# Optimization experiments

Measured on AMD Instinct MI355X. Metric: run time of the kernel, lower is better.

The kernel has to match this reference:

```python
import jax, jax.numpy as jnp
import numpy as np

D_MODEL = 128
D_STATE = 16
D_CONV = 2
EXPAND = 2
D_INNER = EXPAND * D_MODEL  # 256
DT_RANK = (D_MODEL + 15) // 16  # 8
GROUPS = 4
EPS = 1e-5


def setup_inputs() -> dict:
    key = jax.random.key(0)
    ks = jax.random.split(key, 12)
    s = lambda k, shape, sc=0.02: jax.random.normal(k, shape, dtype=jnp.float32) * sc
    inp = {
        "x_hsi": jax.random.normal(ks[0], (8, D_MODEL, 64, 64), dtype=jnp.float32),
        "W_in": s(ks[1], (D_MODEL, 2 * D_INNER)),            # in_proj (no bias)
        "conv_w": s(ks[2], (D_INNER, D_CONV), 0.5),          # depthwise causal conv, k=2
        "conv_b": s(ks[3], (D_INNER,), 0.1),
        "W_x": s(ks[4], (D_INNER, DT_RANK + 2 * D_STATE)),   # x_proj (no bias)
        "W_dt": s(ks[5], (DT_RANK, D_INNER), 0.1),
        "b_dt": s(ks[6], (D_INNER,), 0.1),
        "A_log": jnp.log(jnp.broadcast_to(jnp.arange(1, D_STATE + 1, dtype=jnp.float32), (D_INNER, D_STATE))),
        "D": jnp.ones((D_INNER,), dtype=jnp.float32),
        "W_out": s(ks[7], (D_INNER, D_MODEL)),               # out_proj (no bias)
        "gn_gamma": jnp.ones((D_MODEL,), dtype=jnp.float32),
        "gn_beta": jnp.zeros((D_MODEL,), dtype=jnp.float32),
    }
    return inp


def _causal_conv_k2(x, w, b):
    # x: [B, L, Din]; w: [Din, 2]; causal depthwise conv, kernel size 2
    xp = jnp.pad(x, ((0, 0), (1, 0), (0, 0)))
    return xp[:, :-1] * w[:, 0] + xp[:, 1:] * w[:, 1] + b


def _selective_scan(xc, dt, Bmat, Cmat, A, D):
    # xc,dt: [B,L,Din]; Bmat,Cmat: [B,L,N]; A: [Din,N]; D: [Din]
    def step(h, inp):
        dt_t, B_t, C_t, x_t = inp          # [B,Din],[B,N],[B,N],[B,Din]
        dA = jnp.exp(dt_t[..., None] * A)                      # [B,Din,N]
        dBx = dt_t[..., None] * B_t[:, None, :] * x_t[..., None]
        h = dA * h + dBx
        y = jnp.einsum('bdn,bn->bd', h, C_t)
        return h, y

    B_, L, Din = xc.shape
    h0 = jnp.zeros((B_, Din, A.shape[1]), dtype=xc.dtype)
    xs = (jnp.swapaxes(dt, 0, 1), jnp.swapaxes(Bmat, 0, 1),
          jnp.swapaxes(Cmat, 0, 1), jnp.swapaxes(xc, 0, 1))
    _, ys = jax.lax.scan(step, h0, xs)     # ys: [L,B,Din]
    return jnp.swapaxes(ys, 0, 1) + xc * D


def _mamba(x, W_in, conv_w, conv_b, W_x, W_dt, b_dt, A_log, D, W_out):
    # x: [B, L, d_model]
    xz = x @ W_in                                   # [B,L,2*Din]
    xh, z = jnp.split(xz, 2, axis=-1)
    xh = jax.nn.silu(_causal_conv_k2(xh, conv_w, conv_b))
    x_dbl = xh @ W_x                                # [B,L,dt_rank+2N]
    dt_low = x_dbl[..., :DT_RANK]
    Bmat = x_dbl[..., DT_RANK:DT_RANK + D_STATE]
    Cmat = x_dbl[..., DT_RANK + D_STATE:]
    dt = jax.nn.softplus(dt_low @ W_dt + b_dt)      # [B,L,Din]
    A = -jnp.exp(A_log)
    y = _selective_scan(xh, dt, Bmat, Cmat, A, D)
    y = y * jax.nn.silu(z)
    return y @ W_out


def _group_norm(x, gamma, beta):
    # x: [B,C,H,W]
    B_, C, H, W = x.shape
    xr = x.reshape(B_, GROUPS, -1)
    mean = xr.mean(-1, keepdims=True)
    var = xr.var(-1, keepdims=True)
    xn = ((xr - mean) * jax.lax.rsqrt(var + EPS)).reshape(B_, C, H, W)
    return xn * gamma[:, None, None] + beta[:, None, None]


def reference(x_hsi, W_in, conv_w, conv_b, W_x, W_dt, b_dt, A_log, D, W_out, gn_gamma, gn_beta):
    B_, C, H, W = x_hsi.shape
    x = jnp.transpose(x_hsi, (0, 2, 3, 1)).reshape(B_, H * W, C)
    x = _mamba(x, W_in, conv_w, conv_b, W_x, W_dt, b_dt, A_log, D, W_out)
    x = jnp.transpose(x.reshape(B_, H, W, C), (0, 3, 1, 2))
    x = jax.nn.silu(_group_norm(x, gn_gamma, gn_beta))
    return x + x_hsi
```

## Files before the change

### kernel.cpp

```cpp
#include <hip/hip_runtime.h>
#include <hip/hip_bf16.h>
#include <hip/hip_fp16.h>
#include <math.h>

#define BATCH   8
#define LSEQ    4096
#define CMODEL  128
#define DIN     256
#define NSTATE  16
#define RRANK   8
#define NCH     128
#define TCH     32

typedef __attribute__((ext_vector_type(8))) short short8;
typedef __attribute__((ext_vector_type(4))) float f32x4;
typedef __attribute__((ext_vector_type(2))) float f32x2;

__device__ __forceinline__ float sigmoid_fast(float x) {
    return __builtin_amdgcn_rcpf(1.0f + __expf(-x));
}
__device__ __forceinline__ float silu_fast(float x) { return x * sigmoid_fast(x); }
__device__ __forceinline__ float softplus_fast(float x) {
    return fmaxf(x, 0.0f) + __logf(1.0f + __expf(-fabsf(x)));
}
__device__ __forceinline__ float bf2f(unsigned short u) {
    return __uint_as_float(((unsigned)u) << 16);
}
__device__ __forceinline__ unsigned pk2bf(float a, float b) {
    __hip_bfloat162 t = __float22bfloat162_rn(make_float2(a, b));
    unsigned r;
    __builtin_memcpy(&r, &t, 4);
    return r;
}
__device__ __forceinline__ unsigned short f2bf1(float v) {
    return (unsigned short)pk2bf(v, v);
}

__device__ __forceinline__ void dA_powers2(float dtv, const float* A, bool fast,
                                           f32x2* dA2)
{
    if (fast) {
        float e1 = __expf(dtv * A[0]);
        float e2 = e1 * e1;
        dA2[0] = (f32x2){e1, e2};
        f32x2 e2s = (f32x2){e2, e2};
        #pragma unroll
        for (int j = 1; j < 8; ++j) dA2[j] = dA2[j-1] * e2s;
    } else {
        #pragma unroll
        for (int j = 0; j < 8; ++j)
            dA2[j] = (f32x2){__expf(dtv * A[2*j]), __expf(dtv * A[2*j+1])};
    }
}

#define LSTR 72
#define YSTR 264

__device__ __forceinline__ void tr64_bf(const float* __restrict__ src, int lds,
                                        int r0, int c0,
                                        unsigned short* __restrict__ dst, int ldd)
{
    __shared__ float ts[64][65];
    const int tid = threadIdx.x;
    #pragma unroll
    for (int it = 0; it < 4; ++it) {
        int slot = tid + it * 256;
        int i = slot >> 4, j4 = slot & 15;
        float4 v = *(const float4*)&src[(size_t)(r0 + i) * lds + c0 + j4 * 4];
        ts[i][j4*4+0] = v.x; ts[i][j4*4+1] = v.y;
        ts[i][j4*4+2] = v.z; ts[i][j4*4+3] = v.w;
    }
    __syncthreads();
    #pragma unroll
    for (int it = 0; it < 4; ++it) {
        int slot = tid + it * 256;
        int row = slot >> 4, c4 = slot & 15;
        unsigned p0 = pk2bf(ts[c4*4+0][row], ts[c4*4+1][row]);
        unsigned p1 = pk2bf(ts[c4*4+2][row], ts[c4*4+3][row]);
        unsigned long long u = (unsigned long long)p0 | ((unsigned long long)p1 << 32);
        *(unsigned long long*)&dst[(size_t)(c0 + row) * ldd + r0 + c4 * 4] = u;
    }
}

__global__ __launch_bounds__(256) void k0_setup(
    const float* __restrict__ W_in, const float* __restrict__ W_out,
    const float* __restrict__ W_x,
    unsigned short* __restrict__ wtin, unsigned short* __restrict__ wtout,
    unsigned short* __restrict__ wxt, float* __restrict__ part)
{
    const int bid = blockIdx.x;
    if (bid < 16) {
        int ct = bid >> 3, jt = bid & 7;
        tr64_bf(W_in, 512, ct * 64, jt * 64, wtin, 128);
    } else if (bid < 24) {
        int t3 = bid - 16;
        int kt = t3 >> 1, ct = t3 & 1;
        tr64_bf(W_out, 128, kt * 64, ct * 64, wtout, 256);
    } else if (bid == 24) {
        for (int idx = threadIdx.x; idx < 48 * 256; idx += 256) {
            int j = idx >> 8, k = idx & 255;
            float v = (j < 40) ? W_x[k * 40 + j] : 0.0f;
            wxt[(size_t)j * 256 + k] = f2bf1(v);
        }
    } else {
        if (threadIdx.x < 64) part[threadIdx.x] = 0.0f;
    }
}

__global__ __launch_bounds__(512) void k1_gemm_in(
    const float* __restrict__ x_hsi, const unsigned short* __restrict__ wtin,
    unsigned short* __restrict__ xhbf, unsigned short* __restrict__ zbf)
{
    __shared__ __align__(16) unsigned short Abf[128 * LSTR];
    const int tid = threadIdx.x;
    const int R0  = blockIdx.x * 128;
    const int b   = R0 >> 12;
    const int l0  = R0 & 4095;
    const int jbase = blockIdx.y * 256;

    const int w    = tid >> 6;
    const int lane = tid & 63;
    const int lm   = lane & 15;
    const int q    = lane >> 4;
    const int mbase = (w & 1) * 64;
    const int nbase = (w >> 1) * 64;

    f32x4 acc[4][4];
    #pragma unroll
    for (int i = 0; i < 4; ++i)
        #pragma unroll
        for (int j = 0; j < 4; ++j) acc[i][j] = (f32x4){0.f, 0.f, 0.f, 0.f};

    const int cq = tid & 15;
    const int lq = tid >> 4;

    for (int kc = 0; kc < 128; kc += 64) {
        __syncthreads();
        {
            float v[4][4];
            #pragma unroll
            for (int t = 0; t < 4; ++t) {
                float4 f = *(const float4*)&x_hsi[((b * 128 + kc + cq * 4 + t) << 12) + l0 + lq * 4];
                v[t][0] = f.x; v[t][1] = f.y; v[t][2] = f.z; v[t][3] = f.w;
            }
            #pragma unroll
            for (int i = 0; i < 4; ++i) {
                unsigned p0 = pk2bf(v[0][i], v[1][i]);
                unsigned p1 = pk2bf(v[2][i], v[3][i]);
                unsigned long long u = (unsigned long long)p0 | ((unsigned long long)p1 << 32);
                *(unsigned long long*)&Abf[(lq * 4 + i) * LSTR + cq * 4] = u;
            }
        }
        __syncthreads();
        #pragma unroll
        for (int kt = 0; kt < 2; ++kt) {
            short8 af[4], bfr[4];
            #pragma unroll
            for (int mt = 0; mt < 4; ++mt)
                af[mt] = *(const short8*)&Abf[(mbase + mt * 16 + lm) * LSTR + kt * 32 + q * 8];
            #pragma unroll
            for (int nt = 0; nt < 4; ++nt)
                bfr[nt] = *(const short8*)&wtin[(size_t)(jbase + nbase + nt * 16 + lm) * 128 + kc + kt * 32 + q * 8];
            #pragma unroll
            for (int mt = 0; mt < 4; ++mt)
                #pragma unroll
                for (int nt = 0; nt < 4; ++nt)
                    acc[mt][nt] = __builtin_amdgcn_mfma_f32_16x16x32_bf16(
                        af[mt], bfr[nt], acc[mt][nt], 0, 0, 0);
        }
    }

    const bool is_xh = (jbase == 0);
    #pragma unroll
    for (int mt = 0; mt < 4; ++mt) {
        #pragma unroll
        for (int r = 0; r < 4; ++r) {
            int row = R0 + mbase + mt * 16 + q * 4 + r;
            #pragma unroll
            for (int nt = 0; nt < 4; ++nt) {
                int col = nbase + nt * 16 + lm;
                float val = acc[mt][nt][r];
                if (is_xh) xhbf[row * 256 + col] = f2bf1(val);
                else       zbf[row * 256 + col]  = f2bf1(silu_fast(val));
            }
        }
    }
}

__global__ __launch_bounds__(256) void k46_conv_gemm_scan1(
    const unsigned short* __restrict__ xhbf, const float* __restrict__ conv_w,
    const float* __restrict__ conv_b, const unsigned short* __restrict__ wxt,
    const float* __restrict__ W_dt, const float* __restrict__ b_dt,
    const float* __restrict__ A_log,
    float* __restrict__ xdbl, unsigned short* __restrict__ xcbf,
    float* __restrict__ hend, float* __restrict__ dtsg)
{
    __shared__ float cw0[256], cw1[256], cbs[256];
    __shared__ __align__(16) unsigned short xcb[TCH][YSTR];
    __shared__ __align__(16) float xdl[TCH * 40];
    const int tid = threadIdx.x;
    const int chunk = blockIdx.x;
    const int b = blockIdx.y;
    const int R0 = b * LSEQ + chunk * TCH;

    cw0[tid] = conv_w[2 * tid];
    cw1[tid] = conv_w[2 * tid + 1];
    cbs[tid] = conv_b[tid];

    const int d = tid;
    float A[16];
    #pragma unroll
    for (int qq = 0; qq < 4; ++qq) {
        float4 al = *(const float4*)&A_log[d * 16 + qq * 4];
        A[qq*4+0] = -__expf(al.x); A[qq*4+1] = -__expf(al.y);
        A[qq*4+2] = -__expf(al.z); A[qq*4+3] = -__expf(al.w);
    }
    bool fast = true;
    #pragma unroll
    for (int n = 1; n < 16; ++n)
        fast = fast && (fabsf(A[n] - (n + 1) * A[0]) <= 1e-4f * fabsf(A[n]) + 1e-7f);
    float wdt[8];
    #pragma unroll
    for (int r = 0; r < 8; ++r) wdt[r] = W_dt[r * 256 + d];
    const float bdt = b_dt[d];

    __syncthreads();

    #pragma unroll
    for (int it = 0; it < 8; ++it) {
        int idx = tid + it * 256;
        int r = idx >> 6, qq = idx & 63;
        int row = R0 + r;
        int dd = qq * 4;
        ushort4 cu = *(const ushort4*)&xhbf[(size_t)row * 256 + dd];
        float cur[4] = {bf2f(cu.x), bf2f(cu.y), bf2f(cu.z), bf2f(cu.w)};
        float pv[4] = {0.f, 0.f, 0.f, 0.f};
        if ((row & 4095) != 0) {
            ushort4 pu = *(const ushort4*)&xhbf[(size_t)(row - 1) * 256 + dd];
            pv[0] = bf2f(pu.x); pv[1] = bf2f(pu.y);
            pv[2] = bf2f(pu.z); pv[3] = bf2f(pu.w);
        }
        float o[4];
        #pragma unroll
        for (int e = 0; e < 4; ++e)
            o[e] = silu_fast(pv[e] * cw0[dd+e] + cur[e] * cw1[dd+e] + cbs[dd+e]);
        unsigned p0 = pk2bf(o[0], o[1]), p1 = pk2bf(o[2], o[3]);
        unsigned long long u = (unsigned long long)p0 | ((unsigned long long)p1 << 32);
        *(unsigned long long*)&xcb[r][dd] = u;
        *(unsigned long long*)&xcbf[(size_t)row * 256 + dd] = u;
    }
    __syncthreads();

    const int w    = tid >> 6;
    const int lane = tid & 63;
    const int lm   = lane & 15;
    const int q    = lane >> 4;
    {
        const int mt  = w & 1;
        const int nlo = (w < 2) ? 0 : 2;
        const int nn  = (w < 2) ? 2 : 1;
        f32x4 macc[2];
        macc[0] = (f32x4){0.f,0.f,0.f,0.f};
        macc[1] = (f32x4){0.f,0.f,0.f,0.f};
        for (int kc = 0; kc < 256; kc += 32) {
            short8 af = *(const short8*)&xcb[mt * 16 + lm][kc + q * 8];
            #pragma unroll
            for (int t = 0; t < 2; ++t) {
                if (t < nn) {
                    short8 bfr = *(const short8*)&wxt[(size_t)((nlo + t) * 16 + lm) * 256 + kc + q * 8];
                    macc[t] = __builtin_amdgcn_mfma_f32_16x16x32_bf16(
                        af, bfr, macc[t], 0, 0, 0);
                }
            }
        }
        #pragma unroll
        for (int t = 0; t < 2; ++t) {
            if (t < nn) {
                #pragma unroll
                for (int r = 0; r < 4; ++r) {
                    int row = mt * 16 + q * 4 + r;
                    int col = (nlo + t) * 16 + lm;
                    if (col < 40) {
                        float v = macc[t][r];
                        xdl[row * 40 + col] = v;
                        xdbl[(size_t)(R0 + row) * 40 + col] = v;
                    }
                }
            }
        }
    }
    __syncthreads();

    f32x2 h2[8];
    #pragma unroll
    for (int j = 0; j < 8; ++j) h2[j] = (f32x2){0.f, 0.f};
    float dtsum = 0.f;

    #pragma unroll 2
    for (int tt = 0; tt < TCH; ++tt) {
        float xcv = bf2f(xcb[tt][d]);

        float dl[8];
        *(float4*)&dl[0] = *(const float4*)&xdl[tt * 40 + 0];
        *(float4*)&dl[4] = *(const float4*)&xdl[tt * 40 + 4];
        float dtr = bdt;
        #pragma unroll
        for (int r = 0; r < 8; ++r) dtr = fmaf(dl[r], wdt[r], dtr);
        float dtv = softplus_fast(dtr);
        dtsum += dtv;
        float dtx = dtv * xcv;

        float Bv[16];
        *(float4*)&Bv[0]  = *(const float4*)&xdl[tt * 40 + 8];
        *(float4*)&Bv[4]  = *(const float4*)&xdl[tt * 40 + 12];
        *(float4*)&Bv[8]  = *(const float4*)&xdl[tt * 40 + 16];
        *(float4*)&Bv[12] = *(const float4*)&xdl[tt * 40 + 20];

        f32x2 dA2[8];
        dA_powers2(dtv, A, fast, dA2);
        f32x2 dtx2 = (f32x2){dtx, dtx};
        #pragma unroll
        for (int j = 0; j < 8; ++j) {
            f32x2 Bt2 = (f32x2){Bv[2*j], Bv[2*j+1]};
            h2[j] = dA2[j] * h2[j] + dtx2 * Bt2;
        }
    }

    const float* hf = (const float*)h2;
    const int base = ((b * NCH + chunk) * 256 + d) * 16;
    #pragma unroll
    for (int qq = 0; qq < 4; ++qq)
        *(float4*)&hend[base + qq * 4] = make_float4(hf[qq*4], hf[qq*4+1], hf[qq*4+2], hf[qq*4+3]);
    dtsg[(b * NCH + chunk) * 256 + d] = dtsum;
}

__global__ __launch_bounds__(256) void k7_combine(
    const float* __restrict__ dtsg, const float* __restrict__ A_log,
    float* __restrict__ hx)
{
    const int idx = blockIdx.x * 256 + threadIdx.x;
    const int b = idx >> 12;
    const int rem = idx & 4095;
    const int d = rem >> 4, n = rem & 15;
    const float An = -__expf(A_log[d * 16 + n]);
    const int base = b * NCH * 4096 + rem;
    const int sbase = b * NCH * 256 + d;
    float h = 0.f;
    float Sb[8], Eb[8];
    #pragma unroll
    for (int j = 0; j < 8; ++j) {
        Sb[j] = dtsg[sbase + j * 256];
        Eb[j] = hx[base + j * 4096];
    }
    for (int g = 0; g < NCH / 8; ++g) {
        const int o  = base + g * 32768;
        const int so = sbase + g * 2048;
        float Sn[8] = {0,0,0,0,0,0,0,0}, En[8] = {0,0,0,0,0,0,0,0};
        if (g < NCH / 8 - 1) {
            #pragma unroll
            for (int j = 0; j < 8; ++j) {
                Sn[j] = dtsg[so + 2048 + j * 256];
                En[j] = hx[o + 32768 + j * 4096];
            }
        }
        #pragma unroll
        for (int j = 0; j < 8; ++j) {
            hx[o + j * 4096] = h;
            float P = __expf(Sb[j] * An);
            h = fmaf(P, h, Eb[j]);
        }
        #pragma unroll
        for (int j = 0; j < 8; ++j) { Sb[j] = Sn[j]; Eb[j] = En[j]; }
    }
}

__global__ __launch_bounds__(256) void k89_scan2_gemm_out(
    const unsigned short* __restrict__ xcbf, const float* __restrict__ xdbl,
    const float* __restrict__ W_dt, const float* __restrict__ b_dt,
    const float* __restrict__ A_log, const float* __restrict__ Dvec,
    const float* __restrict__ hin, const unsigned short* __restrict__ zbf,
    const unsigned short* __restrict__ wtout,
    unsigned short* __restrict__ out_bf, float* __restrict__ part)
{
    __shared__ __align__(16) float xdb[TCH * 40];
    __shared__ __align__(16) unsigned short Ybf[TCH][YSTR];
    __shared__ float pred[8];
    const int tid = threadIdx.x;
    const int chunk = blockIdx.x;
    const int b = blockIdx.y;
    const int t0 = b * LSEQ + chunk * TCH;

    #pragma unroll
    for (int it = 0; it < 2; ++it) {
        int i4 = tid + it * 256;
        if (i4 < 320) ((float4*)xdb)[i4] = ((const float4*)&xdbl[(size_t)t0 * 40])[i4];
    }
    if (tid < 8) pred[tid] = 0.0f;

    const int d = tid;
    float A[16];
    #pragma unroll
    for (int qq = 0; qq < 4; ++qq) {
        float4 al = *(const float4*)&A_log[d * 16 + qq * 4];
        A[qq*4+0] = -__expf(al.x); A[qq*4+1] = -__expf(al.y);
        A[qq*4+2] = -__expf(al.z); A[qq*4+3] = -__expf(al.w);
    }
    bool fast = true;
    #pragma unroll
    for (int n = 1; n < 16; ++n)
        fast = fast && (fabsf(A[n] - (n + 1) * A[0]) <= 1e-4f * fabsf(A[n]) + 1e-7f);
    float wdt[8];
    #pragma unroll
    for (int r = 0; r < 8; ++r) wdt[r] = W_dt[r * 256 + d];
    const float bdt = b_dt[d];
    const float Dd = Dvec[d];

    f32x2 h2[8];
    {
        const int hbase = ((b * NCH + chunk) * 256 + d) * 16;
        float hf[16];
        #pragma unroll
        for (int qq = 0; qq < 4; ++qq) {
            float4 hv = *(const float4*)&hin[hbase + qq * 4];
            hf[qq*4+0] = hv.x; hf[qq*4+1] = hv.y; hf[qq*4+2] = hv.z; hf[qq*4+3] = hv.w;
        }
        #pragma unroll
        for (int j = 0; j < 8; ++j) h2[j] = (f32x2){hf[2*j], hf[2*j+1]};
    }
    __syncthreads();

    #pragma unroll 2
    for (int tt = 0; tt < TCH; ++tt) {
        const size_t gi = (size_t)(t0 + tt) * 256 + d;
        float xcv = bf2f(xcbf[gi]);

        float dl[8];
        *(float4*)&dl[0] = *(const float4*)&xdb[tt * 40 + 0];
        *(float4*)&dl[4] = *(const float4*)&xdb[tt * 40 + 4];
        float dtr = bdt;
        #pragma unroll
        for (int r = 0; r < 8; ++r) dtr = fmaf(dl[r], wdt[r], dtr);
        float dtv = softplus_fast(dtr);
        float dtx = dtv * xcv;

        float Bv[16], Cv[16];
        *(float4*)&Bv[0]  = *(const float4*)&xdb[tt * 40 + 8];
        *(float4*)&Bv[4]  = *(const float4*)&xdb[tt * 40 + 12];
        *(float4*)&Bv[8]  = *(const float4*)&xdb[tt * 40 + 16];
        *(float4*)&Bv[12] = *(const float4*)&xdb[tt * 40 + 20];
        *(float4*)&Cv[0]  = *(const float4*)&xdb[tt * 40 + 24];
        *(float4*)&Cv[4]  = *(const float4*)&xdb[tt * 40 + 28];
        *(float4*)&Cv[8]  = *(const float4*)&xdb[tt * 40 + 32];
        *(float4*)&Cv[12] = *(const float4*)&xdb[tt * 40 + 36];

        f32x2 dA2[8];
        dA_powers2(dtv, A, fast, dA2);
        f32x2 dtx2 = (f32x2){dtx, dtx};
        f32x2 yv2 = (f32x2){0.f, 0.f};
        #pragma unroll
        for (int j = 0; j < 8; ++j) {
            f32x2 Bt2 = (f32x2){Bv[2*j], Bv[2*j+1]};
            f32x2 Ct2 = (f32x2){Cv[2*j], Cv[2*j+1]};
            h2[j] = dA2[j] * h2[j] + dtx2 * Bt2;
            yv2 = yv2 + h2[j] * Ct2;
        }
        float yv = yv2.x + yv2.y;
        yv = fmaf(Dd, xcv, yv);
        Ybf[tt][d] = f2bf1(yv * bf2f(zbf[gi]));
    }
    __syncthreads();

    const int w    = tid >> 6;
    const int lane = tid & 63;
    const int lm   = lane & 15;
    const int q    = lane >> 4;
    const int mbase = (w & 1) * 64;
    const int nbase = (w >> 1) * 16;

    f32x4 acc[4];
    #pragma unroll
    for (int i = 0; i < 4; ++i) acc[i] = (f32x4){0.f, 0.f, 0.f, 0.f};

    for (int ks = 0; ks < 256; ks += 32) {
        short8 bfr = *(const short8*)&Ybf[nbase + lm][ks + q * 8];
        #pragma unroll
        for (int mt = 0; mt < 4; ++mt) {
            short8 af = *(const short8*)&wtout[(size_t)(mbase + mt * 16 + lm) * 256 + ks + q * 8];
            acc[mt] = __builtin_amdgcn_mfma_f32_16x16x32_bf16(
                af, bfr, acc[mt], 0, 0, 0);
        }
    }

    const int l0 = chunk * TCH;
    #pragma unroll
    for (int mt = 0; mt < 4; ++mt) {
        #pragma unroll
        for (int r = 0; r < 4; ++r) {
            int c = mbase + mt * 16 + q * 4 + r;
            long obase = (long)(b * 128 + c) * 4096 + l0;
            out_bf[obase + nbase + lm] = f2bf1(acc[mt][r]);
        }
    }

    float s0 = 0.f, q0 = 0.f, s1 = 0.f, q1 = 0.f;
    #pragma unroll
    for (int mt = 0; mt < 4; ++mt)
        #pragma unroll
        for (int r = 0; r < 4; ++r) {
            float v = acc[mt][r];
            if (mt < 2) { s0 += v; q0 += v * v; }
            else        { s1 += v; q1 += v * v; }
        }
    #pragma unroll
    for (int off = 32; off > 0; off >>= 1) {
        s0 += __shfl_down(s0, off, 64);
        q0 += __shfl_down(q0, off, 64);
        s1 += __shfl_down(s1, off, 64);
        q1 += __shfl_down(q1, off, 64);
    }
    if (lane == 0) {
        int g0 = mbase >> 5;
        atomicAdd(&pred[g0 * 2],           s0);
        atomicAdd(&pred[g0 * 2 + 1],       q0);
        atomicAdd(&pred[(g0 + 1) * 2],     s1);
        atomicAdd(&pred[(g0 + 1) * 2 + 1], q1);
    }
    __syncthreads();
    if (tid < 8) atomicAdd(&part[b * 8 + tid], pred[tid]);
}

__global__ __launch_bounds__(256) void k10c_apply(
    const unsigned short* __restrict__ out_bf, const float* __restrict__ part,
    const float* __restrict__ gamma, const float* __restrict__ beta,
    const float* __restrict__ x_hsi, float* __restrict__ out)
{
    __shared__ float sstat[64];
    if (threadIdx.x < 32) {
        float S = part[threadIdx.x * 2];
        float Q = part[threadIdx.x * 2 + 1];
        const float inv_n = 1.0f / 131072.0f;
        float mean = S * inv_n;
        float var  = Q * inv_n - mean * mean;
        sstat[threadIdx.x * 2]     = mean;
        sstat[threadIdx.x * 2 + 1] = rsqrtf(var + 1e-5f);
    }
    __syncthreads();
    const int idx4 = blockIdx.x * 256 + threadIdx.x;
    const int flat = idx4 * 4;
    const int c = (flat >> 12) & 127;
    const int b = flat >> 19;
    const int g = c >> 5;
    const float mean = sstat[(b * 4 + g) * 2];
    const float inv  = sstat[(b * 4 + g) * 2 + 1];
    const float ga = gamma[c], be = beta[c];
    ushort4 u = *(const ushort4*)&out_bf[flat];
    float4 r = *(const float4*)&x_hsi[flat];
    float vv[4] = {bf2f(u.x), bf2f(u.y), bf2f(u.z), bf2f(u.w)};
    float rr[4] = {r.x, r.y, r.z, r.w};
    float o[4];
    #pragma unroll
    for (int qq = 0; qq < 4; ++qq) {
        float xn = (vv[qq] - mean) * inv;
        float gv = xn * ga + be;
        o[qq] = silu_fast(gv) + rr[qq];
    }
    *(float4*)&out[flat] = make_float4(o[0], o[1], o[2], o[3]);
}

extern "C" void kernel_launch(void* const* d_in, const int* in_sizes, int n_in,
                              void* d_out, int out_size, void* d_ws, size_t ws_size,
                              hipStream_t stream)
{
    const float* x_hsi  = (const float*)d_in[0];
    const float* W_in   = (const float*)d_in[1];
    const float* conv_w = (const float*)d_in[2];
    const float* conv_b = (const float*)d_in[3];
    const float* W_x    = (const float*)d_in[4];
    const float* W_dt   = (const float*)d_in[5];
    const float* b_dt   = (const float*)d_in[6];
    const float* A_log  = (const float*)d_in[7];
    const float* Dv     = (const float*)d_in[8];
    const float* W_out  = (const float*)d_in[9];
    const float* gnw    = (const float*)d_in[10];
    const float* gnb    = (const float*)d_in[11];

    float* ws = (float*)d_ws;
    unsigned short* xhbf = (unsigned short*)(ws + 0);
    unsigned short* zbf  = (unsigned short*)(ws + 4194304);
    float* xdbl   = ws + 8388608;
    float* hx     = ws + 8716288;
    float* dtsg   = ws + 12910592;
    unsigned short* xcbf   = (unsigned short*)(ws + 13172736);
    unsigned short* out_bf = (unsigned short*)(ws + 17367040);
    float* part   = ws + 19464192;
    unsigned short* wtin  = (unsigned short*)(ws + 19464256);
    unsigned short* wtout = (unsigned short*)(ws + 19497024);
    unsigned short* wxt   = (unsigned short*)(ws + 19513408);
    float* outp   = (float*)d_out;

    k0_setup<<<26, 256, 0, stream>>>(W_in, W_out, W_x, wtin, wtout, wxt, part);
    k1_gemm_in<<<dim3(256, 2), 512, 0, stream>>>(x_hsi, wtin, xhbf, zbf);
    k46_conv_gemm_scan1<<<dim3(NCH, BATCH), 256, 0, stream>>>(
        xhbf, conv_w, conv_b, wxt, W_dt, b_dt, A_log, xdbl, xcbf, hx, dtsg);
    k7_combine<<<128, 256, 0, stream>>>(dtsg, A_log, hx);
    k89_scan2_gemm_out<<<dim3(NCH, BATCH), 256, 0, stream>>>(
        xcbf, xdbl, W_dt, b_dt, A_log, Dv, hx, zbf, wtout, out_bf, part);
    k10c_apply<<<4096, 256, 0, stream>>>(out_bf, part, gnw, gnb, x_hsi, outp);
}
```

Before: 200.1 us.

## Split conv/x_proj from chunk scan and read xdbl directly from global

Splits the fused conv+x_proj+scan1 kernel into two kernels, one for conv and x_proj, one for the chunk-local scan. Both scan kernels now read per-step dt/B/C rows straight from global memory (broadcast loads), with no shared-memory staging or barrier. This lowers shared-memory use and register pressure per kernel, which may raise occupancy. In exchange it adds a kernel launch and re-reads xcbf and xdbl from global/L2.

```diff
diff --git a/kernel.cpp b/kernel.cpp
--- a/kernel.cpp
+++ b/kernel.cpp
@@ -187,17 +187,13 @@
     }
 }
 
-__global__ __launch_bounds__(256) void k46_conv_gemm_scan1(
+__global__ __launch_bounds__(256) void k46_conv_xdbl(
     const unsigned short* __restrict__ xhbf, const float* __restrict__ conv_w,
     const float* __restrict__ conv_b, const unsigned short* __restrict__ wxt,
-    const float* __restrict__ W_dt, const float* __restrict__ b_dt,
-    const float* __restrict__ A_log,
-    float* __restrict__ xdbl, unsigned short* __restrict__ xcbf,
-    float* __restrict__ hend, float* __restrict__ dtsg)
+    float* __restrict__ xdbl, unsigned short* __restrict__ xcbf)
 {
     __shared__ float cw0[256], cw1[256], cbs[256];
     __shared__ __align__(16) unsigned short xcb[TCH][YSTR];
-    __shared__ __align__(16) float xdl[TCH * 40];
     const int tid = threadIdx.x;
     const int chunk = blockIdx.x;
     const int b = blockIdx.y;
@@ -206,24 +202,6 @@
     cw0[tid] = conv_w[2 * tid];
     cw1[tid] = conv_w[2 * tid + 1];
     cbs[tid] = conv_b[tid];
-
-    const int d = tid;
-    float A[16];
-    #pragma unroll
-    for (int qq = 0; qq < 4; ++qq) {
-        float4 al = *(const float4*)&A_log[d * 16 + qq * 4];
-        A[qq*4+0] = -__expf(al.x); A[qq*4+1] = -__expf(al.y);
-        A[qq*4+2] = -__expf(al.z); A[qq*4+3] = -__expf(al.w);
-    }
-    bool fast = true;
-    #pragma unroll
-    for (int n = 1; n < 16; ++n)
-        fast = fast && (fabsf(A[n] - (n + 1) * A[0]) <= 1e-4f * fabsf(A[n]) + 1e-7f);
-    float wdt[8];
-    #pragma unroll
-    for (int r = 0; r < 8; ++r) wdt[r] = W_dt[r * 256 + d];
-    const float bdt = b_dt[d];
-
     __syncthreads();
 
     #pragma unroll
@@ -255,41 +233,63 @@
     const int lane = tid & 63;
     const int lm   = lane & 15;
     const int q    = lane >> 4;
-    {
-        const int mt  = w & 1;
-        const int nlo = (w < 2) ? 0 : 2;
-        const int nn  = (w < 2) ? 2 : 1;
-        f32x4 macc[2];
-        macc[0] = (f32x4){0.f,0.f,0.f,0.f};
-        macc[1] = (f32x4){0.f,0.f,0.f,0.f};
-        for (int kc = 0; kc < 256; kc += 32) {
-            short8 af = *(const short8*)&xcb[mt * 16 + lm][kc + q * 8];
-            #pragma unroll
-            for (int t = 0; t < 2; ++t) {
-                if (t < nn) {
-                    short8 bfr = *(const short8*)&wxt[(size_t)((nlo + t) * 16 + lm) * 256 + kc + q * 8];
-                    macc[t] = __builtin_amdgcn_mfma_f32_16x16x32_bf16(
-                        af, bfr, macc[t], 0, 0, 0);
-                }
-            }
-        }
+    const int mt  = w & 1;
+    const int nlo = (w < 2) ? 0 : 2;
+    const int nn  = (w < 2) ? 2 : 1;
+    f32x4 macc[2];
+    macc[0] = (f32x4){0.f,0.f,0.f,0.f};
+    macc[1] = (f32x4){0.f,0.f,0.f,0.f};
+    for (int kc = 0; kc < 256; kc += 32) {
+        short8 af = *(const short8*)&xcb[mt * 16 + lm][kc + q * 8];
         #pragma unroll
         for (int t = 0; t < 2; ++t) {
             if (t < nn) {
-                #pragma unroll
-                for (int r = 0; r < 4; ++r) {
-                    int row = mt * 16 + q * 4 + r;
-                    int col = (nlo + t) * 16 + lm;
-                    if (col < 40) {
-                        float v = macc[t][r];
-                        xdl[row * 40 + col] = v;
-                        xdbl[(size_t)(R0 + row) * 40 + col] = v;
-                    }
-                }
+                short8 bfr = *(const short8*)&wxt[(size_t)((nlo + t) * 16 + lm) * 256 + kc + q * 8];
+                macc[t] = __builtin_amdgcn_mfma_f32_16x16x32_bf16(
+                    af, bfr, macc[t], 0, 0, 0);
             }
         }
     }
-    __syncthreads();
+    #pragma unroll
+    for (int t = 0; t < 2; ++t) {
+        if (t < nn) {
+            #pragma unroll
+            for (int r = 0; r < 4; ++r) {
+                int row = mt * 16 + q * 4 + r;
+                int col = (nlo + t) * 16 + lm;
+                if (col < 40)
+                    xdbl[(size_t)(R0 + row) * 40 + col] = macc[t][r];
+            }
+        }
+    }
+}
+
+__global__ __launch_bounds__(256) void k6_scan1(
+    const unsigned short* __restrict__ xcbf, const float* __restrict__ xdbl,
+    const float* __restrict__ W_dt, const float* __restrict__ b_dt,
+    const float* __restrict__ A_log,
+    float* __restrict__ hend, float* __restrict__ dtsg)
+{
+    const int d = threadIdx.x;
+    const int chunk = blockIdx.x;
+    const int b = blockIdx.y;
+    const int t0 = b * LSEQ + chunk * TCH;
+
+    float A[16];
+    #pragma unroll
+    for (int qq = 0; qq < 4; ++qq) {
+        float4 al = *(const float4*)&A_log[d * 16 + qq * 4];
+        A[qq*4+0] = -__expf(al.x); A[qq*4+1] = -__expf(al.y);
+        A[qq*4+2] = -__expf(al.z); A[qq*4+3] = -__expf(al.w);
+    }
+    bool fast = true;
+    #pragma unroll
+    for (int n = 1; n < 16; ++n)
+        fast = fast && (fabsf(A[n] - (n + 1) * A[0]) <= 1e-4f * fabsf(A[n]) + 1e-7f);
+    float wdt[8];
+    #pragma unroll
+    for (int r = 0; r < 8; ++r) wdt[r] = W_dt[r * 256 + d];
+    const float bdt = b_dt[d];
 
     f32x2 h2[8];
     #pragma unroll
@@ -298,23 +298,24 @@
 
     #pragma unroll 2
     for (int tt = 0; tt < TCH; ++tt) {
-        float xcv = bf2f(xcb[tt][d]);
-
-        float dl[8];
-        *(float4*)&dl[0] = *(const float4*)&xdl[tt * 40 + 0];
-        *(float4*)&dl[4] = *(const float4*)&xdl[tt * 40 + 4];
+        const int row = t0 + tt;
+        float xcv = bf2f(xcbf[(size_t)row * 256 + d]);
+
+        const float* xr = &xdbl[(size_t)row * 40];
+        float dl[8], Bv[16];
+        *(float4*)&dl[0] = *(const float4*)&xr[0];
+        *(float4*)&dl[4] = *(const float4*)&xr[4];
+        *(float4*)&Bv[0]  = *(const float4*)&xr[8];
+        *(float4*)&Bv[4]  = *(const float4*)&xr[12];
+        *(float4*)&Bv[8]  = *(const float4*)&xr[16];
+        *(float4*)&Bv[12] = *(const float4*)&xr[20];
+
         float dtr = bdt;
         #pragma unroll
         for (int r = 0; r < 8; ++r) dtr = fmaf(dl[r], wdt[r], dtr);
         float dtv = softplus_fast(dtr);
         dtsum += dtv;
         float dtx = dtv * xcv;
-
-        float Bv[16];
-        *(float4*)&Bv[0]  = *(const float4*)&xdl[tt * 40 + 8];
-        *(float4*)&Bv[4]  = *(const float4*)&xdl[tt * 40 + 12];
-        *(float4*)&Bv[8]  = *(const float4*)&xdl[tt * 40 + 16];
-        *(float4*)&Bv[12] = *(const float4*)&xdl[tt * 40 + 20];
 
         f32x2 dA2[8];
         dA_powers2(dtv, A, fast, dA2);
@@ -382,7 +383,6 @@
     const unsigned short* __restrict__ wtout,
     unsigned short* __restrict__ out_bf, float* __restrict__ part)
 {
-    __shared__ __align__(16) float xdb[TCH * 40];
     __shared__ __align__(16) unsigned short Ybf[TCH][YSTR];
     __shared__ float pred[8];
     const int tid = threadIdx.x;
@@ -390,11 +390,6 @@
     const int b = blockIdx.y;
     const int t0 = b * LSEQ + chunk * TCH;
 
-    #pragma unroll
-    for (int it = 0; it < 2; ++it) {
-        int i4 = tid + it * 256;
-        if (i4 < 320) ((float4*)xdb)[i4] = ((const float4*)&xdbl[(size_t)t0 * 40])[i4];
-    }
     if (tid < 8) pred[tid] = 0.0f;
 
     const int d = tid;
@@ -427,31 +422,31 @@
         #pragma unroll
         for (int j = 0; j < 8; ++j) h2[j] = (f32x2){hf[2*j], hf[2*j+1]};
     }
-    __syncthreads();
 
     #pragma unroll 2
     for (int tt = 0; tt < TCH; ++tt) {
-        const size_t gi = (size_t)(t0 + tt) * 256 + d;
+        const int row = t0 + tt;
+        const size_t gi = (size_t)row * 256 + d;
         float xcv = bf2f(xcbf[gi]);
 
-        float dl[8];
-        *(float4*)&dl[0] = *(const float4*)&xdb[tt * 40 + 0];
-        *(float4*)&dl[4] = *(const float4*)&xdb[tt * 40 + 4];
+        const float* xr = &xdbl[(size_t)row * 40];
+        float dl[8], Bv[16], Cv[16];
+        *(float4*)&dl[0] = *(const float4*)&xr[0];
+        *(float4*)&dl[4] = *(const float4*)&xr[4];
+        *(float4*)&Bv[0]  = *(const float4*)&xr[8];
+        *(float4*)&Bv[4]  = *(const float4*)&xr[12];
+        *(float4*)&Bv[8]  = *(const float4*)&xr[16];
+        *(float4*)&Bv[12] = *(const float4*)&xr[20];
+        *(float4*)&Cv[0]  = *(const float4*)&xr[24];
+        *(float4*)&Cv[4]  = *(const float4*)&xr[28];
+        *(float4*)&Cv[8]  = *(const float4*)&xr[32];
+        *(float4*)&Cv[12] = *(const float4*)&xr[36];
+
         float dtr = bdt;
         #pragma unroll
         for (int r = 0; r < 8; ++r) dtr = fmaf(dl[r], wdt[r], dtr);
         float dtv = softplus_fast(dtr);
         float dtx = dtv * xcv;
-
-        float Bv[16], Cv[16];
-        *(float4*)&Bv[0]  = *(const float4*)&xdb[tt * 40 + 8];
-        *(float4*)&Bv[4]  = *(const float4*)&xdb[tt * 40 + 12];
-        *(float4*)&Bv[8]  = *(const float4*)&xdb[tt * 40 + 16];
-        *(float4*)&Bv[12] = *(const float4*)&xdb[tt * 40 + 20];
-        *(float4*)&Cv[0]  = *(const float4*)&xdb[tt * 40 + 24];
-        *(float4*)&Cv[4]  = *(const float4*)&xdb[tt * 40 + 28];
-        *(float4*)&Cv[8]  = *(const float4*)&xdb[tt * 40 + 32];
-        *(float4*)&Cv[12] = *(const float4*)&xdb[tt * 40 + 36];
 
         f32x2 dA2[8];
         dA_powers2(dtv, A, fast, dA2);
@@ -600,8 +595,10 @@
 
     k0_setup<<<26, 256, 0, stream>>>(W_in, W_out, W_x, wtin, wtout, wxt, part);
     k1_gemm_in<<<dim3(256, 2), 512, 0, stream>>>(x_hsi, wtin, xhbf, zbf);
-    k46_conv_gemm_scan1<<<dim3(NCH, BATCH), 256, 0, stream>>>(
-        xhbf, conv_w, conv_b, wxt, W_dt, b_dt, A_log, xdbl, xcbf, hx, dtsg);
+    k46_conv_xdbl<<<dim3(NCH, BATCH), 256, 0, stream>>>(
+        xhbf, conv_w, conv_b, wxt, xdbl, xcbf);
+    k6_scan1<<<dim3(NCH, BATCH), 256, 0, stream>>>(
+        xcbf, xdbl, W_dt, b_dt, A_log, hx, dtsg);
     k7_combine<<<128, 256, 0, stream>>>(dtsg, A_log, hx);
     k89_scan2_gemm_out<<<dim3(NCH, BATCH), 256, 0, stream>>>(
         xcbf, xdbl, W_dt, b_dt, A_log, Dv, hx, zbf, wtout, out_bf, part);
```

After: 206.0 us. 3.0% more time.
